# Kernel tuning notes

Measured on AMD Instinct MI355X. Metric: run time of the kernel, lower is better.

Reference implementation:

```python
import jax, jax.numpy as jnp
import numpy as np

IN_SIZE = 224
KERNEL = 5
STRIDE = 1
IN_CH = 16
OUT_CH = 64
LAMB = 5.0
LR = 0.005
GAMMA = 0.99
EPS_ = 0.01
NH = (IN_SIZE - KERNEL) // STRIDE + 1          # 220 output positions per side
NB_TILES = NH * NH                              # 48400 tiles


def setup_inputs() -> dict:
    key = jax.random.key(0)
    k1, k2 = jax.random.split(key)
    x = jax.random.normal(k1, (1, IN_CH, IN_SIZE, IN_SIZE), dtype=jnp.float32)
    # torch.nn.init.uniform_(param, a=0, b=1)
    W = jax.random.uniform(k2, (OUT_CH, IN_CH, KERNEL, KERNEL), dtype=jnp.float32)
    exp_avg = jnp.zeros((OUT_CH,), dtype=jnp.float32)
    return {"x": x, "W": W, "exp_avg": exp_avg, "clamped": 0}


def _inhibition(out):
    out = jax.nn.relu(out)
    m = jnp.max(out, axis=1, keepdims=True)     # max over channel dim
    out = out / (m + 1e-9)
    return out ** LAMB


def _flatten_input(x):
    # mirrors x.unfold(2,k,s).unfold(3,k,s) -> [T, C*k*k] with (C, kh, kw) ordering
    starts = jnp.arange(NH) * STRIDE
    rows = starts[:, None] + jnp.arange(KERNEL)  # [NH, K]
    p = x[0][:, rows]                            # [C, NH, K, W]
    p = p[:, :, :, rows]                         # [C, NH, K, NH, K]
    p = p.transpose(1, 3, 0, 2, 4)               # [NH, NH, C, K, K]
    return p.reshape(NB_TILES, -1)               # [T, D]


def reference(x, W, exp_avg, clamped):
    # forward conv + inhibition
    out = jax.lax.conv_general_dilated(
        x, W, (STRIDE, STRIDE), 'VALID',
        dimension_numbers=('NCHW', 'OIHW', 'NCHW'))
    out = _inhibition(out)                       # [1, O, NH, NH]

    # Hebbian FullyOrthogonal update (no-grad buffer update in the original)
    y = out[0].transpose(1, 2, 0).reshape(-1, OUT_CH)   # [T, O]
    xf = _flatten_input(x)                               # [T, D]
    Wf = W.reshape(OUT_CH, -1)                           # [O, D]
    # mean_t( lr * (y_t (x) x_t - y_t (x) (y_t W)) ) = lr/T * (Y^T X - (Y^T Y) W)
    yty = y.T @ y                                        # [O, O]
    avg_delta = (LR / NB_TILES) * (y.T @ xf - yty @ Wf)  # [O, D]
    Wnew = jax.nn.relu(Wf + avg_delta).reshape(OUT_CH, IN_CH, KERNEL, KERNEL)
    exp_new = GAMMA * exp_avg + (1.0 - GAMMA) * jnp.mean(y, axis=0)

    # weight decay scaling
    A = exp_new / jnp.mean(exp_new)
    gfp = EPS_ * jnp.tanh(-EPS_ * (A - 1.0)) + 1.0
    gfn = 1.0 / gfp
    pos = jnp.where(Wnew > 0, Wnew, 0.0) * gfp.reshape(-1, 1, 1, 1)
    neg = jnp.where(Wnew < 0, Wnew, 0.0) * gfn.reshape(-1, 1, 1, 1)
    Wfinal = pos + neg
    return out, Wfinal, exp_new
```

## Files before the change

### kernel.cpp

```cpp
#include <hip/hip_runtime.h>
#include <stdint.h>

#define IN_SIZE 224
#define KER 5
#define IN_CH 16
#define OUT_CH 64
#define NH 220
#define NB_TILES (NH * NH)
#define XCH (IN_SIZE * IN_SIZE)
#define OUT_PLANE NB_TILES
#define KP2 51200
#define XS 52224
#define XTROWS 50304
#define LR_OVER_NB ((float)(0.005 / 48400.0))
#define GAMMA_F 0.99f
#define ONE_MINUS_GAMMA 0.01f
#define EPS_F 0.01f

#define NCHUNK 64
#define CK 800
#define PSTRIDE (64 * 512)

typedef __attribute__((ext_vector_type(8))) short short8;
typedef __attribute__((ext_vector_type(4))) float floatx4;

__device__ inline uint16_t f2bf(float f) {
    uint32_t u = __float_as_uint(f);
    return (uint16_t)((u + 0x7FFFu + ((u >> 16) & 1u)) >> 16);
}
__device__ inline float bf2f(uint16_t h) { return __uint_as_float((uint32_t)h << 16); }

__global__ __launch_bounds__(256) void prepa_kernel(const float* __restrict__ x,
                                                    uint16_t* __restrict__ xth,
                                                    uint16_t* __restrict__ xtl,
                                                    const float* __restrict__ W,
                                                    uint16_t* __restrict__ wrh,
                                                    uint16_t* __restrict__ wrl) {
    int blk = blockIdx.x;
    if (blk < 197) {
        int addr = blk * 256 + threadIdx.x;
        if (addr >= XTROWS) return;
        uint32_t dh[8], dl[8];
        if (addr < XCH) {
#pragma unroll
            for (int q = 0; q < 8; q++) {
                float v0 = x[(2 * q) * XCH + addr];
                float v1 = x[(2 * q + 1) * XCH + addr];
                uint16_t h0 = f2bf(v0), h1 = f2bf(v1);
                uint16_t l0 = f2bf(v0 - bf2f(h0)), l1 = f2bf(v1 - bf2f(h1));
                dh[q] = (uint32_t)h0 | ((uint32_t)h1 << 16);
                dl[q] = (uint32_t)l0 | ((uint32_t)l1 << 16);
            }
        } else {
#pragma unroll
            for (int q = 0; q < 8; q++) { dh[q] = 0u; dl[q] = 0u; }
        }
        *(uint4*)(xth + addr * 16) = make_uint4(dh[0], dh[1], dh[2], dh[3]);
        *(uint4*)(xth + addr * 16 + 8) = make_uint4(dh[4], dh[5], dh[6], dh[7]);
        *(uint4*)(xtl + addr * 16) = make_uint4(dl[0], dl[1], dl[2], dl[3]);
        *(uint4*)(xtl + addr * 16 + 8) = make_uint4(dl[4], dl[5], dl[6], dl[7]);
    } else {
        int idx = (blk - 197) * 256 + threadIdx.x;
        if (idx >= 13 * 4 * 64 * 8) return;
        int j = idx & 7;
        int lane = (idx >> 3) & 63;
        int ocg = (idx >> 9) & 3;
        int t = idx >> 11;
        int k = (lane >> 4) * 8 + j;
        int s = k >> 4, c = k & 15;
        int oc = 16 * ocg + (lane & 15);
        int tap = 2 * t + s;
        float v = (tap < 25) ? W[oc * 400 + c * 25 + tap] : 0.f;
        uint16_t h = f2bf(v);
        wrh[idx] = h;
        wrl[idx] = f2bf(v - bf2f(h));
    }
}

__global__ __launch_bounds__(256) void conv_prep_kernel(const uint16_t* __restrict__ xth,
                                                        const uint16_t* __restrict__ xtl,
                                                        const uint16_t* __restrict__ wrh,
                                                        const uint16_t* __restrict__ wrl,
                                                        float* __restrict__ out,
                                                        uint16_t* __restrict__ yb,
                                                        const float* __restrict__ x,
                                                        uint16_t* __restrict__ xs,
                                                        uint16_t* __restrict__ ones) {
    if (blockIdx.x >= 770) {
        int t = (blockIdx.x - 770) * 256 + threadIdx.x;
        const int perq = XS / 4;
        if (t < 5 * 16 * perq) {
            int kj = t / (16 * perq);
            int rem = t - kj * (16 * perq);
            int c = rem / perq;
            int q = (rem - c * perq) * 4;
            int base = c * XCH;
            ushort4 o;
            int i0 = q + kj;     o.x = f2bf(x[base + (i0 < XCH ? i0 : XCH - 1)]);
            int i1 = q + kj + 1; o.y = f2bf(x[base + (i1 < XCH ? i1 : XCH - 1)]);
            int i2 = q + kj + 2; o.z = f2bf(x[base + (i2 < XCH ? i2 : XCH - 1)]);
            int i3 = q + kj + 3; o.w = f2bf(x[base + (i3 < XCH ? i3 : XCH - 1)]);
            *(ushort4*)(xs + (kj * 16 + c) * XS + q) = o;
        }
        ushort4 z = {0, 0, 0, 0};
        if (t < 64 * 480) {
            int r = t / 480, q = (t - r * 480) * 4;
            *(ushort4*)(yb + r * KP2 + 49280 + q) = z;
        }
        if (t < 64 * 220) {
            int o = t / 220, i = t - o * 220;
            *(ushort4*)(yb + o * KP2 + i * 224 + 220) = z;
        }
        if (t < 12816) {
            ushort4 o1 = {0x3F80, 0x3F80, 0x3F80, 0x3F80};
            ((ushort4*)ones)[t] = o1;
        }
        return;
    }

    const int lane = threadIdx.x & 63;
    const int w = threadIdx.x >> 6;
    const int l15 = lane & 15;
    const int quad = lane >> 4;
    const int P0 = blockIdx.x * 64;
    const int c0 = (quad & 1) * 8;
    const int sq = quad >> 1;

    __shared__ uint16_t bsh[5 * 68 * 16];
    __shared__ uint16_t bsl[5 * 68 * 16];
    for (int u = threadIdx.x; u < 680; u += 256) {
        int row = u >> 1;
        int half = (u & 1) * 8;
        int strip = row / 68;
        int rr = row - strip * 68;
        int grow = P0 + strip * 224 + rr;
        *(uint4*)(bsh + row * 16 + half) = *(const uint4*)(xth + grow * 16 + half);
        *(uint4*)(bsl + row * 16 + half) = *(const uint4*)(xtl + grow * 16 + half);
    }
    __syncthreads();

    floatx4 acc[4];
#pragma unroll
    for (int g = 0; g < 4; g++) acc[g] = (floatx4){0.f, 0.f, 0.f, 0.f};

#pragma unroll
    for (int t = 0; t < 13; t++) {
        short8 ah = *(const short8*)(wrh + ((t * 4 + w) * 64 + lane) * 8);
        short8 al = *(const short8*)(wrl + ((t * 4 + w) * 64 + lane) * 8);
        const int tap0 = 2 * t, tap1 = 2 * t + 1;
        const int ki0 = tap0 / 5, kj0 = tap0 % 5;
        const int ki1 = (tap1 <= 24) ? tap1 / 5 : 0;
        const int kj1 = (tap1 <= 24) ? tap1 % 5 : 0;
        const int strip = sq ? ki1 : ki0;
        const int kjv = sq ? kj1 : kj0;
#pragma unroll
        for (int g = 0; g < 4; g++) {
            int lrow = strip * 68 + 16 * g + l15 + kjv;
            short8 bh = *(const short8*)(bsh + lrow * 16 + c0);
            short8 bl = *(const short8*)(bsl + lrow * 16 + c0);
            acc[g] = __builtin_amdgcn_mfma_f32_16x16x32_bf16(ah, bh, acc[g], 0, 0, 0);
            acc[g] = __builtin_amdgcn_mfma_f32_16x16x32_bf16(ah, bl, acc[g], 0, 0, 0);
            acc[g] = __builtin_amdgcn_mfma_f32_16x16x32_bf16(al, bh, acc[g], 0, 0, 0);
        }
    }

    __shared__ float wmax[4][64];
    float pmax[4];
#pragma unroll
    for (int g = 0; g < 4; g++) {
        float mx = fmaxf(fmaxf(acc[g][0], acc[g][1]), fmaxf(acc[g][2], acc[g][3]));
        mx = fmaxf(mx, 0.f);
        mx = fmaxf(mx, __shfl_xor(mx, 16));
        mx = fmaxf(mx, __shfl_xor(mx, 32));
        pmax[g] = mx;
    }
    if (quad == 0) {
#pragma unroll
        for (int g = 0; g < 4; g++) wmax[w][g * 16 + l15] = pmax[g];
    }
    __syncthreads();

#pragma unroll
    for (int g = 0; g < 4; g++) {
        int P = P0 + 16 * g + l15;
        int i = P / 224;
        int j = P - i * 224;
        bool valid = j < NH;
        float mx = fmaxf(fmaxf(wmax[0][g * 16 + l15], wmax[1][g * 16 + l15]),
                         fmaxf(wmax[2][g * 16 + l15], wmax[3][g * 16 + l15]));
        float inv = 1.f / (mx + 1e-9f);
#pragma unroll
        for (int r = 0; r < 4; r++) {
            float tv = fmaxf(acc[g][r], 0.f) * inv;
            float t2 = tv * tv;
            tv = t2 * t2 * tv;
            if (valid) {
                int oc = 16 * w + quad * 4 + r;
                out[oc * OUT_PLANE + i * NH + j] = tv;
                yb[oc * KP2 + P] = f2bf(tv);
            }
        }
    }
}

__global__ __launch_bounds__(256) void gemm_kernel(const uint16_t* __restrict__ yb,
                                                   const uint16_t* __restrict__ xs,
                                                   const uint16_t* __restrict__ ones,
                                                   float* __restrict__ Mpart) {
    __shared__ uint16_t As[2][64 * 40];
    __shared__ uint16_t Bs[2][64 * 40];
    const int tid = threadIdx.x;
    const int lane = tid & 63;
    const int w = tid >> 6;
    const int l15 = lane & 15;
    const int quad = lane >> 4;
    const int kg = quad * 8;
    const int b = blockIdx.x;
    const int xcd = b & 7;
    const int t8 = b >> 3;
    const int ntile = t8 & 7;
    const int chunk = xcd + 8 * (t8 >> 3);
    const int k0 = chunk * CK;

    const int sr = tid >> 2;
    const int sseg = (tid & 3) * 8;
    const uint16_t* pa = yb + sr * KP2 + k0 + sseg;

    int n_g = ntile * 64 + sr;
    const uint16_t* pbase;
    if (n_g < 400) {
        int c = n_g / 25;
        int r = n_g - 25 * c;
        int ki = r / 5;
        int kj = r - 5 * ki;
        pbase = xs + (kj * 16 + c) * XS + ki * 224;
    } else if (n_g < 464) {
        pbase = yb + (n_g - 400) * KP2;
    } else if (n_g == 464) {
        pbase = ones;
    } else {
        pbase = yb;
    }
    const uint16_t* pb = pbase + k0 + sseg;

    floatx4 acc[4];
#pragma unroll
    for (int i = 0; i < 4; i++) acc[i] = (floatx4){0.f, 0.f, 0.f, 0.f};

    uint4 ra = *(const uint4*)pa;
    uint4 rb = *(const uint4*)pb;

    for (int s = 0; s < 25; s++) {
        const int p = s & 1;
        *(uint4*)&As[p][sr * 40 + sseg] = ra;
        *(uint4*)&Bs[p][sr * 40 + sseg] = rb;
        __syncthreads();
        if (s + 1 < 25) {
            pa += 32;
            pb += 32;
            ra = *(const uint4*)pa;
            rb = *(const uint4*)pb;
        }
        short8 af = *(const short8*)&As[p][(16 * w + l15) * 40 + kg];
#pragma unroll
        for (int ng = 0; ng < 4; ng++) {
            short8 bf = *(const short8*)&Bs[p][(16 * ng + l15) * 40 + kg];
            acc[ng] = __builtin_amdgcn_mfma_f32_16x16x32_bf16(af, bf, acc[ng], 0, 0, 0);
        }
        __syncthreads();
    }

    float* dst = Mpart + chunk * PSTRIDE;
#pragma unroll
    for (int ng = 0; ng < 4; ng++) {
        int col = ntile * 64 + ng * 16 + l15;
        if (col < 465) {
#pragma unroll
            for (int r = 0; r < 4; r++)
                dst[(16 * w + quad * 4 + r) * 512 + col] = acc[ng][r];
        }
    }
}

__global__ __launch_bounds__(256) void finalize_w_kernel(const float* __restrict__ W,
                                                         const float* __restrict__ Mpart,
                                                         const float* __restrict__ exp_avg,
                                                         float* __restrict__ Wout,
                                                         float* __restrict__ expout) {
    __shared__ float gfps[OUT_CH];
    __shared__ float ytys[2][OUT_CH];
    const int tid = threadIdx.x;
    const int bid = blockIdx.x;
    const int first_o = (bid * 256) / 400;

    if (tid < OUT_CH) {
        int o = tid;
        float cs = 0.f;
#pragma unroll 8
        for (int ch = 0; ch < NCHUNK; ch++) cs += Mpart[ch * PSTRIDE + o * 512 + 464];
        float e = GAMMA_F * exp_avg[o] + ONE_MINUS_GAMMA * (cs / (float)NB_TILES);
        float s = e;
        for (int off = 32; off; off >>= 1) s += __shfl_down(s, off);
        s = __shfl(s, 0);
        float A = e / (s / (float)OUT_CH);
        gfps[o] = EPS_F * tanhf(-EPS_F * (A - 1.f)) + 1.f;
        if (bid == 0) expout[o] = e;
    }
    if (tid >= 128) {
        int t = tid - 128;
        int orow = first_o + (t >> 6);
        int k = t & 63;
        float s = 0.f;
        if (orow < OUT_CH) {
#pragma unroll 8
            for (int ch = 0; ch < NCHUNK; ch++) s += Mpart[ch * PSTRIDE + orow * 512 + 400 + k];
        }
        ytys[t >> 6][k] = s;
    }
    __syncthreads();

    int idx = bid * 256 + tid;
    int o = idx / 400;
    int q = idx - o * 400;
    float Mv = 0.f;
#pragma unroll 8
    for (int ch = 0; ch < NCHUNK; ch++) Mv += Mpart[ch * PSTRIDE + o * 512 + q];
    const float* yrow = ytys[o - first_o];
    float dot = 0.f;
#pragma unroll 8
    for (int k = 0; k < OUT_CH; k++) dot = fmaf(yrow[k], W[k * 400 + q], dot);
    float wv = W[idx] + LR_OVER_NB * (Mv - dot);
    wv = fmaxf(wv, 0.f);
    float gp = gfps[o];
    float pos = (wv > 0.f ? wv : 0.f) * gp;
    float neg = (wv < 0.f ? wv : 0.f) / gp;
    Wout[idx] = pos + neg;
}

extern "C" void kernel_launch(void* const* d_in, const int* in_sizes, int n_in,
                              void* d_out, int out_size, void* d_ws, size_t ws_size,
                              hipStream_t stream) {
    const float* x = (const float*)d_in[0];
    const float* W = (const float*)d_in[1];
    const float* exp_avg = (const float*)d_in[2];
    float* out = (float*)d_out;

    float* wsf = (float*)d_ws;
    float* Mpart = wsf + 29760;
    uint16_t* xth = (uint16_t*)Mpart;
    uint16_t* xtl = xth + XTROWS * 16;
    uint16_t* wrh = xtl + XTROWS * 16;
    uint16_t* wrl = wrh + 26624;
    uint16_t* ybf = (uint16_t*)(wsf + 29760 + NCHUNK * PSTRIDE);
    uint16_t* xsb = ybf + OUT_CH * KP2;
    uint16_t* ones = xsb + 5 * 16 * XS;

    float* Wout = out + OUT_CH * OUT_PLANE;
    float* expout = Wout + OUT_CH * IN_CH * KER * KER;

    prepa_kernel<<<301, 256, 0, stream>>>(x, xth, xtl, W, wrh, wrl);
    conv_prep_kernel<<<770 + 4080, 256, 0, stream>>>(xth, xtl, wrh, wrl, out, ybf, x, xsb, ones);
    gemm_kernel<<<512, 256, 0, stream>>>(ybf, xsb, ones, Mpart);
    finalize_w_kernel<<<100, 256, 0, stream>>>(W, Mpart, exp_avg, Wout, expout);
}
```

Baseline: 110.4 us.

## Load GEMM MFMA fragments directly from global memory, dropping LDS staging

```diff
diff --git a/kernel.cpp b/kernel.cpp
--- a/kernel.cpp
+++ b/kernel.cpp
@@ -207,14 +207,11 @@
                                                    const uint16_t* __restrict__ xs,
                                                    const uint16_t* __restrict__ ones,
                                                    float* __restrict__ Mpart) {
-    __shared__ uint16_t As[2][64 * 40];
-    __shared__ uint16_t Bs[2][64 * 40];
     const int tid = threadIdx.x;
     const int lane = tid & 63;
     const int w = tid >> 6;
     const int l15 = lane & 15;
     const int quad = lane >> 4;
-    const int kg = quad * 8;
     const int b = blockIdx.x;
     const int xcd = b & 7;
     const int t8 = b >> 3;
@@ -222,52 +219,66 @@
     const int chunk = xcd + 8 * (t8 >> 3);
     const int k0 = chunk * CK;
 
-    const int sr = tid >> 2;
-    const int sseg = (tid & 3) * 8;
-    const uint16_t* pa = yb + sr * KP2 + k0 + sseg;
-
-    int n_g = ntile * 64 + sr;
-    const uint16_t* pbase;
-    if (n_g < 400) {
-        int c = n_g / 25;
-        int r = n_g - 25 * c;
-        int ki = r / 5;
-        int kj = r - 5 * ki;
-        pbase = xs + (kj * 16 + c) * XS + ki * 224;
-    } else if (n_g < 464) {
-        pbase = yb + (n_g - 400) * KP2;
-    } else if (n_g == 464) {
-        pbase = ones;
-    } else {
-        pbase = yb;
-    }
-    const uint16_t* pb = pbase + k0 + sseg;
+    const uint16_t* pa = yb + (16 * w + l15) * KP2 + k0 + quad * 8;
+
+    const uint16_t* pb0;
+    const uint16_t* pb1;
+    const uint16_t* pb2;
+    const uint16_t* pb3;
+#pragma unroll
+    for (int ng = 0; ng < 4; ng++) {
+        int n_g = ntile * 64 + 16 * ng + l15;
+        const uint16_t* pbase;
+        if (n_g < 400) {
+            int c = n_g / 25;
+            int r = n_g - 25 * c;
+            int ki = r / 5;
+            int kj = r - 5 * ki;
+            pbase = xs + (kj * 16 + c) * XS + ki * 224;
+        } else if (n_g < 464) {
+            pbase = yb + (n_g - 400) * KP2;
+        } else if (n_g == 464) {
+            pbase = ones;
+        } else {
+            pbase = yb;
+        }
+        const uint16_t* p = pbase + k0 + quad * 8;
+        if (ng == 0) pb0 = p;
+        else if (ng == 1) pb1 = p;
+        else if (ng == 2) pb2 = p;
+        else pb3 = p;
+    }
 
     floatx4 acc[4];
 #pragma unroll
     for (int i = 0; i < 4; i++) acc[i] = (floatx4){0.f, 0.f, 0.f, 0.f};
 
-    uint4 ra = *(const uint4*)pa;
-    uint4 rb = *(const uint4*)pb;
-
+    short8 ca = *(const short8*)(pa);
+    short8 cb0 = *(const short8*)(pb0);
+    short8 cb1 = *(const short8*)(pb1);
+    short8 cb2 = *(const short8*)(pb2);
+    short8 cb3 = *(const short8*)(pb3);
+    short8 na = *(const short8*)(pa + 32);
+    short8 nb0 = *(const short8*)(pb0 + 32);
+    short8 nb1 = *(const short8*)(pb1 + 32);
+    short8 nb2 = *(const short8*)(pb2 + 32);
+    short8 nb3 = *(const short8*)(pb3 + 32);
+
+#pragma unroll
     for (int s = 0; s < 25; s++) {
-        const int p = s & 1;
-        *(uint4*)&As[p][sr * 40 + sseg] = ra;
-        *(uint4*)&Bs[p][sr * 40 + sseg] = rb;
-        __syncthreads();
-        if (s + 1 < 25) {
-            pa += 32;
-            pb += 32;
-            ra = *(const uint4*)pa;
-            rb = *(const uint4*)pb;
-        }
-        short8 af = *(const short8*)&As[p][(16 * w + l15) * 40 + kg];
-#pragma unroll
-        for (int ng = 0; ng < 4; ng++) {
-            short8 bf = *(const short8*)&Bs[p][(16 * ng + l15) * 40 + kg];
-            acc[ng] = __builtin_amdgcn_mfma_f32_16x16x32_bf16(af, bf, acc[ng], 0, 0, 0);
-        }
-        __syncthreads();
+        acc[0] = __builtin_amdgcn_mfma_f32_16x16x32_bf16(ca, cb0, acc[0], 0, 0, 0);
+        acc[1] = __builtin_amdgcn_mfma_f32_16x16x32_bf16(ca, cb1, acc[1], 0, 0, 0);
+        acc[2] = __builtin_amdgcn_mfma_f32_16x16x32_bf16(ca, cb2, acc[2], 0, 0, 0);
+        acc[3] = __builtin_amdgcn_mfma_f32_16x16x32_bf16(ca, cb3, acc[3], 0, 0, 0);
+        ca = na; cb0 = nb0; cb1 = nb1; cb2 = nb2; cb3 = nb3;
+        if (s + 2 < 25) {
+            const int off = (s + 2) * 32;
+            na = *(const short8*)(pa + off);
+            nb0 = *(const short8*)(pb0 + off);
+            nb1 = *(const short8*)(pb1 + off);
+            nb2 = *(const short8*)(pb2 + off);
+            nb3 = *(const short8*)(pb3 + off);
+        }
     }
 
     float* dst = Mpart + chunk * PSTRIDE;
```

Result: slower. 125.9 us (+14.0%).

## Fuse x bf16 hi/lo transpose into conv kernel and swizzle LDS tile

Applied to the files above, without the earlier changes.

```diff
diff --git a/kernel.cpp b/kernel.cpp
--- a/kernel.cpp
+++ b/kernel.cpp
@@ -11,7 +11,6 @@
 #define OUT_PLANE NB_TILES
 #define KP2 51200
 #define XS 52224
-#define XTROWS 50304
 #define LR_OVER_NB ((float)(0.005 / 48400.0))
 #define GAMMA_F 0.99f
 #define ONE_MINUS_GAMMA 0.01f
@@ -30,56 +29,26 @@
 }
 __device__ inline float bf2f(uint16_t h) { return __uint_as_float((uint32_t)h << 16); }
 
-__global__ __launch_bounds__(256) void prepa_kernel(const float* __restrict__ x,
-                                                    uint16_t* __restrict__ xth,
-                                                    uint16_t* __restrict__ xtl,
-                                                    const float* __restrict__ W,
+__global__ __launch_bounds__(256) void prepa_kernel(const float* __restrict__ W,
                                                     uint16_t* __restrict__ wrh,
                                                     uint16_t* __restrict__ wrl) {
-    int blk = blockIdx.x;
-    if (blk < 197) {
-        int addr = blk * 256 + threadIdx.x;
-        if (addr >= XTROWS) return;
-        uint32_t dh[8], dl[8];
-        if (addr < XCH) {
-#pragma unroll
-            for (int q = 0; q < 8; q++) {
-                float v0 = x[(2 * q) * XCH + addr];
-                float v1 = x[(2 * q + 1) * XCH + addr];
-                uint16_t h0 = f2bf(v0), h1 = f2bf(v1);
-                uint16_t l0 = f2bf(v0 - bf2f(h0)), l1 = f2bf(v1 - bf2f(h1));
-                dh[q] = (uint32_t)h0 | ((uint32_t)h1 << 16);
-                dl[q] = (uint32_t)l0 | ((uint32_t)l1 << 16);
-            }
-        } else {
-#pragma unroll
-            for (int q = 0; q < 8; q++) { dh[q] = 0u; dl[q] = 0u; }
-        }
-        *(uint4*)(xth + addr * 16) = make_uint4(dh[0], dh[1], dh[2], dh[3]);
-        *(uint4*)(xth + addr * 16 + 8) = make_uint4(dh[4], dh[5], dh[6], dh[7]);
-        *(uint4*)(xtl + addr * 16) = make_uint4(dl[0], dl[1], dl[2], dl[3]);
-        *(uint4*)(xtl + addr * 16 + 8) = make_uint4(dl[4], dl[5], dl[6], dl[7]);
-    } else {
-        int idx = (blk - 197) * 256 + threadIdx.x;
-        if (idx >= 13 * 4 * 64 * 8) return;
-        int j = idx & 7;
-        int lane = (idx >> 3) & 63;
-        int ocg = (idx >> 9) & 3;
-        int t = idx >> 11;
-        int k = (lane >> 4) * 8 + j;
-        int s = k >> 4, c = k & 15;
-        int oc = 16 * ocg + (lane & 15);
-        int tap = 2 * t + s;
-        float v = (tap < 25) ? W[oc * 400 + c * 25 + tap] : 0.f;
-        uint16_t h = f2bf(v);
-        wrh[idx] = h;
-        wrl[idx] = f2bf(v - bf2f(h));
-    }
-}
-
-__global__ __launch_bounds__(256) void conv_prep_kernel(const uint16_t* __restrict__ xth,
-                                                        const uint16_t* __restrict__ xtl,
-                                                        const uint16_t* __restrict__ wrh,
+    int idx = blockIdx.x * 256 + threadIdx.x;
+    if (idx >= 13 * 4 * 64 * 8) return;
+    int j = idx & 7;
+    int lane = (idx >> 3) & 63;
+    int ocg = (idx >> 9) & 3;
+    int t = idx >> 11;
+    int k = (lane >> 4) * 8 + j;
+    int s = k >> 4, c = k & 15;
+    int oc = 16 * ocg + (lane & 15);
+    int tap = 2 * t + s;
+    float v = (tap < 25) ? W[oc * 400 + c * 25 + tap] : 0.f;
+    uint16_t h = f2bf(v);
+    wrh[idx] = h;
+    wrl[idx] = f2bf(v - bf2f(h));
+}
+
+__global__ __launch_bounds__(256) void conv_prep_kernel(const uint16_t* __restrict__ wrh,
                                                         const uint16_t* __restrict__ wrl,
                                                         float* __restrict__ out,
                                                         uint16_t* __restrict__ yb,
@@ -123,19 +92,31 @@
     const int l15 = lane & 15;
     const int quad = lane >> 4;
     const int P0 = blockIdx.x * 64;
-    const int c0 = (quad & 1) * 8;
+    const int chalf = quad & 1;
     const int sq = quad >> 1;
 
     __shared__ uint16_t bsh[5 * 68 * 16];
     __shared__ uint16_t bsl[5 * 68 * 16];
     for (int u = threadIdx.x; u < 680; u += 256) {
         int row = u >> 1;
-        int half = (u & 1) * 8;
+        int half = u & 1;
         int strip = row / 68;
         int rr = row - strip * 68;
         int grow = P0 + strip * 224 + rr;
-        *(uint4*)(bsh + row * 16 + half) = *(const uint4*)(xth + grow * 16 + half);
-        *(uint4*)(bsl + row * 16 + half) = *(const uint4*)(xtl + grow * 16 + half);
+        bool inb = grow < XCH;
+        uint32_t dh[4], dl[4];
+#pragma unroll
+        for (int q = 0; q < 4; q++) {
+            float v0 = inb ? x[(half * 8 + 2 * q) * XCH + grow] : 0.f;
+            float v1 = inb ? x[(half * 8 + 2 * q + 1) * XCH + grow] : 0.f;
+            uint16_t h0 = f2bf(v0), h1 = f2bf(v1);
+            uint16_t l0 = f2bf(v0 - bf2f(h0)), l1 = f2bf(v1 - bf2f(h1));
+            dh[q] = (uint32_t)h0 | ((uint32_t)h1 << 16);
+            dl[q] = (uint32_t)l0 | ((uint32_t)l1 << 16);
+        }
+        int swz = (u ^ ((row >> 2) & 1)) * 8;
+        *(uint4*)(bsh + swz) = make_uint4(dh[0], dh[1], dh[2], dh[3]);
+        *(uint4*)(bsl + swz) = make_uint4(dl[0], dl[1], dl[2], dl[3]);
     }
     __syncthreads();
 
@@ -156,8 +137,10 @@
 #pragma unroll
         for (int g = 0; g < 4; g++) {
             int lrow = strip * 68 + 16 * g + l15 + kjv;
-            short8 bh = *(const short8*)(bsh + lrow * 16 + c0);
-            short8 bl = *(const short8*)(bsl + lrow * 16 + c0);
+            int unit = lrow * 2 + chalf;
+            int off = (unit ^ ((lrow >> 2) & 1)) * 8;
+            short8 bh = *(const short8*)(bsh + off);
+            short8 bl = *(const short8*)(bsl + off);
             acc[g] = __builtin_amdgcn_mfma_f32_16x16x32_bf16(ah, bh, acc[g], 0, 0, 0);
             acc[g] = __builtin_amdgcn_mfma_f32_16x16x32_bf16(ah, bl, acc[g], 0, 0, 0);
             acc[g] = __builtin_amdgcn_mfma_f32_16x16x32_bf16(al, bh, acc[g], 0, 0, 0);
@@ -347,9 +330,7 @@
 
     float* wsf = (float*)d_ws;
     float* Mpart = wsf + 29760;
-    uint16_t* xth = (uint16_t*)Mpart;
-    uint16_t* xtl = xth + XTROWS * 16;
-    uint16_t* wrh = xtl + XTROWS * 16;
+    uint16_t* wrh = (uint16_t*)Mpart;
     uint16_t* wrl = wrh + 26624;
     uint16_t* ybf = (uint16_t*)(wsf + 29760 + NCHUNK * PSTRIDE);
     uint16_t* xsb = ybf + OUT_CH * KP2;
@@ -358,8 +339,8 @@
     float* Wout = out + OUT_CH * OUT_PLANE;
     float* expout = Wout + OUT_CH * IN_CH * KER * KER;
 
-    prepa_kernel<<<301, 256, 0, stream>>>(x, xth, xtl, W, wrh, wrl);
-    conv_prep_kernel<<<770 + 4080, 256, 0, stream>>>(xth, xtl, wrh, wrl, out, ybf, x, xsb, ones);
+    prepa_kernel<<<104, 256, 0, stream>>>(W, wrh, wrl);
+    conv_prep_kernel<<<770 + 4080, 256, 0, stream>>>(wrh, wrl, out, ybf, x, xsb, ones);
     gemm_kernel<<<512, 256, 0, stream>>>(ybf, xsb, ones, Mpart);
     finalize_w_kernel<<<100, 256, 0, stream>>>(W, Mpart, exp_avg, Wout, expout);
 }
```

New measurement: 110.1 us. Within noise of the previous version (-0.2%).
